# Performance work log

Measured on AMD Instinct MI355X. Metric: run time of the kernel, lower is better.

Reference implementation:

```python
import jax, jax.numpy as jnp
import numpy as np

B, T, D_IN, D_PROJ = 256, 2048, 25, 128


def setup_inputs() -> dict:
    key = jax.random.key(0)
    ks = jax.random.split(key, 7)
    s1 = 1.0 / np.sqrt(D_IN)
    s2 = 1.0 / np.sqrt(D_PROJ)
    return {
        "x": jax.random.normal(ks[0], (B, T, D_IN), dtype=jnp.float32),
        "ln_gamma": jnp.ones((D_IN,), dtype=jnp.float32),
        "ln_beta": jnp.zeros((D_IN,), dtype=jnp.float32),
        "w1": jax.random.uniform(ks[1], (D_IN, D_PROJ), jnp.float32, -s1, s1),
        "b1": jax.random.uniform(ks[2], (D_PROJ,), jnp.float32, -s1, s1),
        "w2": jax.random.uniform(ks[3], (D_PROJ, D_PROJ), jnp.float32, -s2, s2),
        "b2": jax.random.uniform(ks[4], (D_PROJ,), jnp.float32, -s2, s2),
    }


def reference(x, ln_gamma, ln_beta, w1, b1, w2, b2):
    # LayerNorm over last dim (eps=1e-5, torch default)
    mu = jnp.mean(x, axis=-1, keepdims=True)
    var = jnp.mean(jnp.square(x - mu), axis=-1, keepdims=True)
    xn = (x - mu) * jax.lax.rsqrt(var + 1e-5) * ln_gamma + ln_beta
    h = jnp.einsum("btd,dp->btp", xn, w1) + b1
    h = jax.nn.gelu(h, approximate=False)  # torch nn.GELU default = exact erf
    return jnp.einsum("btp,pq->btq", h, w2) + b2
```

## Files before the change

kernel.cpp:

```cpp
#include <hip/hip_runtime.h>
#include <hip/hip_bf16.h>
#include <stdint.h>

#define BT    (256*2048)
#define DIN   25
#define DP    128
#define MTILE 128
#define NBLK  (BT/MTILE)
#define BAND  8192
#define XOFF  4992
#define SM_BYTES (4*BAND)

typedef __attribute__((ext_vector_type(8))) __bf16 bf16x8;
typedef __attribute__((ext_vector_type(4))) __bf16 bf16x4;
typedef __attribute__((ext_vector_type(4))) float  f32x4;
typedef __attribute__((ext_vector_type(2))) float  f32x2;

__device__ __forceinline__ unsigned short f2bf(float f) {
  unsigned int u = __float_as_uint(f);
  u += 0x7fffu + ((u >> 16) & 1u);
  return (unsigned short)(u >> 16);
}

__device__ __forceinline__ float gelu_exact(float x) {
  float z  = 0.70710678118654752f * x;
  float az = __builtin_fabsf(z);
  float t  = __builtin_amdgcn_rcpf(1.0f + 0.3275911f * az);
  float p  = t*(0.254829592f + t*(-0.284496736f + t*(1.421413741f +
             t*(-1.453152027f + t*1.061405429f))));
  float e  = __expf(-z*z);
  float erf_az = 1.0f - p*e;
  float erf_z  = (x < 0.f) ? -erf_az : erf_az;
  return 0.5f * x * (1.0f + erf_z);
}

__device__ __forceinline__ void async16(void* lds, const void* g) {
  __builtin_amdgcn_global_load_lds(
      (const __attribute__((address_space(1))) unsigned int*)g,
      (__attribute__((address_space(3)))       unsigned int*)lds, 16, 0, 0);
}

__global__ void prep_kernel(const float* __restrict__ w1, const float* __restrict__ w2,
                            unsigned short* __restrict__ wf) {
  int idx = blockIdx.x * 256 + threadIdx.x;
  if (idx >= 40 * 512) return;
  int f = idx >> 9, r = idx & 511, l = r >> 3, j = r & 7;
  int l15 = l & 15, kq = (l >> 4) * 8 + j;
  float val;
  if (f < 8) {
    int n = (f >> 2) * 64 + l15 * 4 + (f & 3);
    val = (kq < DIN) ? w1[kq * DP + n] : 0.f;
  } else {
    int q = f - 8, F = q >> 2, ks = q & 3;
    int k = ks * 32 + kq;
    int n = (F >> 1) * 32 + l15 * 2 + (F & 1);
    val = w2[k * DP + n];
  }
  wf[idx] = f2bf(val);
}

__global__ __launch_bounds__(256, 3) void fused_kernel(
    const float* __restrict__ x,   const float* __restrict__ gam,
    const float* __restrict__ bet, const float* __restrict__ b1,
    const float* __restrict__ b2,  const unsigned short* __restrict__ wfr,
    float* __restrict__ out) {
  __shared__ __align__(16) unsigned char smem[SM_BYTES];
  const int tid  = threadIdx.x;
  const int lane = tid & 63, w = tid >> 6;
  const int quad = lane >> 4, l15 = lane & 15;
  const int kbase = quad * 8;
  const long long rowW = (long long)blockIdx.x * MTILE + w * 32;
  unsigned char* band = smem + w * BAND;
  const unsigned char* wfb = (const unsigned char*)wfr;

  {
    const unsigned char* src = (const unsigned char*)x + rowW * (DIN * 4);
    for (int c = lane; c < 200; c += 64)
      async16(band + XOFF + c * 16, src + c * 16);
  }

  float gk[8], bk[8];
#pragma unroll
  for (int j = 0; j < 8; j++) {
    int k = kbase + j;
    bool v = (k < DIN);
    gk[j] = v ? gam[k] : 0.f;
    bk[j] = v ? bet[k] : 0.f;
  }
  bf16x8 wb1[8];
#pragma unroll
  for (int f = 0; f < 8; f++)
    wb1[f] = *(const bf16x8*)(wfb + f * 1024 + lane * 16);
  float b1v[8];
#pragma unroll
  for (int f = 0; f < 8; f++)
    b1v[f] = b1[(f >> 2) * 64 + l15 * 4 + (f & 3)];

  asm volatile("s_waitcnt vmcnt(0)" ::: "memory");
  __builtin_amdgcn_sched_barrier(0);

  const float* xs = (const float*)(band + XOFF);
  bf16x8 afrag[2];
#pragma unroll
  for (int t = 0; t < 2; t++) {
    float xv[8];
    float s = 0.f;
#pragma unroll
    for (int j = 0; j < 8; j++) {
      int k = kbase + j;
      float v = 0.f;
      if (k < DIN) v = xs[(t * 16 + l15) * DIN + k];
      xv[j] = v;
      s += v;
    }
    s += __shfl_xor(s, 16);  s += __shfl_xor(s, 32);
    float mu = s * (1.f / DIN);
    float vv = 0.f;
#pragma unroll
    for (int j = 0; j < 8; j++) {
      int k = kbase + j;
      float d = (k < DIN) ? (xv[j] - mu) : 0.f;
      vv += d * d;
    }
    vv += __shfl_xor(vv, 16); vv += __shfl_xor(vv, 32);
    float inv = rsqrtf(vv * (1.f / DIN) + 1e-5f);
    bf16x8 av;
#pragma unroll
    for (int j = 0; j < 8; j++)
      av[j] = (__bf16)((xv[j] - mu) * inv * gk[j] + bk[j]);
    afrag[t] = av;
  }
  asm volatile("s_waitcnt lgkmcnt(0)" ::: "memory");
  __builtin_amdgcn_sched_barrier(0);

  const f32x4 zf = {0.f, 0.f, 0.f, 0.f};
#pragma unroll
  for (int t = 0; t < 2; t++) {
#pragma unroll
    for (int g = 0; g < 2; g++) {
      f32x4 acc[4];
#pragma unroll
      for (int c = 0; c < 4; c++)
        acc[c] = __builtin_amdgcn_mfma_f32_16x16x32_bf16(afrag[t], wb1[g * 4 + c], zf, 0, 0, 0);
#pragma unroll
      for (int r = 0; r < 4; r++) {
        int rl   = t * 16 + quad * 4 + r;
        int swz  = ((quad * 4 + r) & 7) << 4;
        bf16x4 hv;
#pragma unroll
        for (int c = 0; c < 4; c++)
          hv[c] = (__bf16)gelu_exact(acc[c][r] + b1v[g * 4 + c]);
        *(bf16x4*)(band + rl * 256 + ((g * 128 + l15 * 8) ^ swz)) = hv;
      }
    }
  }

  bf16x8 wb2[2][4];
#pragma unroll
  for (int ni = 0; ni < 2; ni++)
#pragma unroll
    for (int ks = 0; ks < 4; ks++)
      wb2[ni][ks] = *(const bf16x8*)(wfb + 8192 + (((w * 2 + ni) * 4) + ks) * 1024 + lane * 16);
  f32x2 bias2 = *(const f32x2*)(b2 + w * 32 + 2 * l15);

  __syncthreads();

  const long long orow0 = (long long)blockIdx.x * MTILE;
  const int rswz = (l15 & 7) << 4;
#pragma unroll
  for (int mt = 0; mt < 8; mt++) {
    bf16x8 af[4];
#pragma unroll
    for (int ks = 0; ks < 4; ks++)
      af[ks] = *(const bf16x8*)(smem + (mt * 16 + l15) * 256 + ((ks * 64 + quad * 16) ^ rswz));
    f32x4 a0 = zf, a1 = zf;
#pragma unroll
    for (int ks = 0; ks < 4; ks++) {
      a0 = __builtin_amdgcn_mfma_f32_16x16x32_bf16(af[ks], wb2[0][ks], a0, 0, 0, 0);
      a1 = __builtin_amdgcn_mfma_f32_16x16x32_bf16(af[ks], wb2[1][ks], a1, 0, 0, 0);
    }
    float* orow = out + (orow0 + mt * 16) * DP + w * 32 + 2 * l15;
#pragma unroll
    for (int r = 0; r < 4; r++) {
      int row = quad * 4 + r;
      f32x2 o; o[0] = a0[r] + bias2[0]; o[1] = a1[r] + bias2[1];
      *(f32x2*)(orow + row * DP) = o;
    }
  }
}

extern "C" void kernel_launch(void* const* d_in, const int* in_sizes, int n_in,
                              void* d_out, int out_size, void* d_ws, size_t ws_size,
                              hipStream_t stream) {
  const float* x   = (const float*)d_in[0];
  const float* gam = (const float*)d_in[1];
  const float* bet = (const float*)d_in[2];
  const float* w1  = (const float*)d_in[3];
  const float* b1  = (const float*)d_in[4];
  const float* w2  = (const float*)d_in[5];
  const float* b2  = (const float*)d_in[6];
  float* out = (float*)d_out;
  unsigned short* wf = (unsigned short*)d_ws;

  prep_kernel<<<80, 256, 0, stream>>>(w1, w2, wf);
  fused_kernel<<<NBLK, 256, 0, stream>>>(x, gam, bet, b1, b2, wf, out);
}
```

Measured before the change: 328.0 us.

## Make fused kernel persistent with double-buffered async x prefetch

Launches a fixed 1024 blocks that each loop over several 128-row tiles. The next tile's x rows are prefetched into a second LDS staging buffer with async global-to-LDS loads while the current tile runs LayerNorm, GEMM1+GELU and GEMM2. This amortizes weight fragment loads and block setup across tiles, and hides x load latency behind compute. In exchange it uses more LDS, lowers the occupancy target from 3 to 2 blocks, and adds two block barriers per tile. The wait relies on a hard-coded vmcnt(4) that must match the number of outstanding loads, including the output stores.

```diff
diff --git a/kernel.cpp b/kernel.cpp
--- a/kernel.cpp
+++ b/kernel.cpp
@@ -6,10 +6,12 @@
 #define DIN   25
 #define DP    128
 #define MTILE 128
-#define NBLK  (BT/MTILE)
-#define BAND  8192
-#define XOFF  4992
-#define SM_BYTES (4*BAND)
+#define NTILE (BT/MTILE)
+#define NBLK  1024
+#define TPB   (NTILE/NBLK)
+#define HBYTES 32768
+#define XSTG   12800
+#define SM_BYTES (HBYTES + 2*XSTG)
 
 typedef __attribute__((ext_vector_type(8))) __bf16 bf16x8;
 typedef __attribute__((ext_vector_type(4))) __bf16 bf16x4;
@@ -59,7 +61,7 @@
   wf[idx] = f2bf(val);
 }
 
-__global__ __launch_bounds__(256, 3) void fused_kernel(
+__global__ __launch_bounds__(256, 2) void fused_kernel(
     const float* __restrict__ x,   const float* __restrict__ gam,
     const float* __restrict__ bet, const float* __restrict__ b1,
     const float* __restrict__ b2,  const unsigned short* __restrict__ wfr,
@@ -69,15 +71,22 @@
   const int lane = tid & 63, w = tid >> 6;
   const int quad = lane >> 4, l15 = lane & 15;
   const int kbase = quad * 8;
-  const long long rowW = (long long)blockIdx.x * MTILE + w * 32;
-  unsigned char* band = smem + w * BAND;
+  const long long tile0 = (long long)blockIdx.x * TPB;
+  unsigned char* band = smem + w * 8192;
   const unsigned char* wfb = (const unsigned char*)wfr;
-
-  {
-    const unsigned char* src = (const unsigned char*)x + rowW * (DIN * 4);
-    for (int c = lane; c < 200; c += 64)
-      async16(band + XOFF + c * 16, src + c * 16);
-  }
+  const unsigned char* xb  = (const unsigned char*)x;
+
+  auto STAGE = [&](int ti, int sbuf) {
+    const unsigned char* src = xb + ((tile0 + ti) * 128LL + w * 32) * 100;
+    unsigned char* dst = smem + HBYTES + sbuf * XSTG + w * 3200;
+#pragma unroll
+    for (int i2 = 0; i2 < 4; i2++) {
+      int c = lane + i2 * 64;
+      if (c < 200) async16(dst + c * 16, src + c * 16);
+    }
+  };
+
+  STAGE(0, 0);
 
   float gk[8], bk[8];
 #pragma unroll
@@ -95,66 +104,6 @@
 #pragma unroll
   for (int f = 0; f < 8; f++)
     b1v[f] = b1[(f >> 2) * 64 + l15 * 4 + (f & 3)];
-
-  asm volatile("s_waitcnt vmcnt(0)" ::: "memory");
-  __builtin_amdgcn_sched_barrier(0);
-
-  const float* xs = (const float*)(band + XOFF);
-  bf16x8 afrag[2];
-#pragma unroll
-  for (int t = 0; t < 2; t++) {
-    float xv[8];
-    float s = 0.f;
-#pragma unroll
-    for (int j = 0; j < 8; j++) {
-      int k = kbase + j;
-      float v = 0.f;
-      if (k < DIN) v = xs[(t * 16 + l15) * DIN + k];
-      xv[j] = v;
-      s += v;
-    }
-    s += __shfl_xor(s, 16);  s += __shfl_xor(s, 32);
-    float mu = s * (1.f / DIN);
-    float vv = 0.f;
-#pragma unroll
-    for (int j = 0; j < 8; j++) {
-      int k = kbase + j;
-      float d = (k < DIN) ? (xv[j] - mu) : 0.f;
-      vv += d * d;
-    }
-    vv += __shfl_xor(vv, 16); vv += __shfl_xor(vv, 32);
-    float inv = rsqrtf(vv * (1.f / DIN) + 1e-5f);
-    bf16x8 av;
-#pragma unroll
-    for (int j = 0; j < 8; j++)
-      av[j] = (__bf16)((xv[j] - mu) * inv * gk[j] + bk[j]);
-    afrag[t] = av;
-  }
-  asm volatile("s_waitcnt lgkmcnt(0)" ::: "memory");
-  __builtin_amdgcn_sched_barrier(0);
-
-  const f32x4 zf = {0.f, 0.f, 0.f, 0.f};
-#pragma unroll
-  for (int t = 0; t < 2; t++) {
-#pragma unroll
-    for (int g = 0; g < 2; g++) {
-      f32x4 acc[4];
-#pragma unroll
-      for (int c = 0; c < 4; c++)
-        acc[c] = __builtin_amdgcn_mfma_f32_16x16x32_bf16(afrag[t], wb1[g * 4 + c], zf, 0, 0, 0);
-#pragma unroll
-      for (int r = 0; r < 4; r++) {
-        int rl   = t * 16 + quad * 4 + r;
-        int swz  = ((quad * 4 + r) & 7) << 4;
-        bf16x4 hv;
-#pragma unroll
-        for (int c = 0; c < 4; c++)
-          hv[c] = (__bf16)gelu_exact(acc[c][r] + b1v[g * 4 + c]);
-        *(bf16x4*)(band + rl * 256 + ((g * 128 + l15 * 8) ^ swz)) = hv;
-      }
-    }
-  }
-
   bf16x8 wb2[2][4];
 #pragma unroll
   for (int ni = 0; ni < 2; ni++)
@@ -163,29 +112,93 @@
       wb2[ni][ks] = *(const bf16x8*)(wfb + 8192 + (((w * 2 + ni) * 4) + ks) * 1024 + lane * 16);
   f32x2 bias2 = *(const f32x2*)(b2 + w * 32 + 2 * l15);
 
-  __syncthreads();
-
-  const long long orow0 = (long long)blockIdx.x * MTILE;
-  const int rswz = (l15 & 7) << 4;
-#pragma unroll
-  for (int mt = 0; mt < 8; mt++) {
-    bf16x8 af[4];
-#pragma unroll
-    for (int ks = 0; ks < 4; ks++)
-      af[ks] = *(const bf16x8*)(smem + (mt * 16 + l15) * 256 + ((ks * 64 + quad * 16) ^ rswz));
-    f32x4 a0 = zf, a1 = zf;
-#pragma unroll
-    for (int ks = 0; ks < 4; ks++) {
-      a0 = __builtin_amdgcn_mfma_f32_16x16x32_bf16(af[ks], wb2[0][ks], a0, 0, 0, 0);
-      a1 = __builtin_amdgcn_mfma_f32_16x16x32_bf16(af[ks], wb2[1][ks], a1, 0, 0, 0);
-    }
-    float* orow = out + (orow0 + mt * 16) * DP + w * 32 + 2 * l15;
-#pragma unroll
-    for (int r = 0; r < 4; r++) {
-      int row = quad * 4 + r;
-      f32x2 o; o[0] = a0[r] + bias2[0]; o[1] = a1[r] + bias2[1];
-      *(f32x2*)(orow + row * DP) = o;
-    }
+  const f32x4 zf = {0.f, 0.f, 0.f, 0.f};
+
+  for (int it = 0; it < TPB; it++) {
+    const int s = it & 1;
+    STAGE((it + 1 < TPB) ? it + 1 : 0, s ^ 1);
+    asm volatile("s_waitcnt vmcnt(4)" ::: "memory");
+    __builtin_amdgcn_sched_barrier(0);
+
+    const float* xs = (const float*)(smem + HBYTES + s * XSTG + w * 3200);
+    bf16x8 afrag[2];
+#pragma unroll
+    for (int t = 0; t < 2; t++) {
+      float xv[8];
+      float sum = 0.f;
+#pragma unroll
+      for (int j = 0; j < 8; j++) {
+        int k = kbase + j;
+        float v = 0.f;
+        if (k < DIN) v = xs[(t * 16 + l15) * DIN + k];
+        xv[j] = v;
+        sum += v;
+      }
+      sum += __shfl_xor(sum, 16);  sum += __shfl_xor(sum, 32);
+      float mu = sum * (1.f / DIN);
+      float vv = 0.f;
+#pragma unroll
+      for (int j = 0; j < 8; j++) {
+        int k = kbase + j;
+        float d = (k < DIN) ? (xv[j] - mu) : 0.f;
+        vv += d * d;
+      }
+      vv += __shfl_xor(vv, 16); vv += __shfl_xor(vv, 32);
+      float inv = rsqrtf(vv * (1.f / DIN) + 1e-5f);
+      bf16x8 av;
+#pragma unroll
+      for (int j = 0; j < 8; j++)
+        av[j] = (__bf16)((xv[j] - mu) * inv * gk[j] + bk[j]);
+      afrag[t] = av;
+    }
+
+#pragma unroll
+    for (int t = 0; t < 2; t++) {
+#pragma unroll
+      for (int cg = 0; cg < 2; cg++) {
+        f32x4 acc[4];
+#pragma unroll
+        for (int c = 0; c < 4; c++)
+          acc[c] = __builtin_amdgcn_mfma_f32_16x16x32_bf16(afrag[t], wb1[cg * 4 + c], zf, 0, 0, 0);
+#pragma unroll
+        for (int r = 0; r < 4; r++) {
+          int rl  = t * 16 + quad * 4 + r;
+          int swz = ((quad * 4 + r) & 7) << 4;
+          bf16x4 hv;
+#pragma unroll
+          for (int c = 0; c < 4; c++)
+            hv[c] = (__bf16)gelu_exact(acc[c][r] + b1v[cg * 4 + c]);
+          *(bf16x4*)(band + rl * 256 + ((cg * 128 + l15 * 8) ^ swz)) = hv;
+        }
+      }
+    }
+
+    __syncthreads();
+
+    const long long orow0 = (tile0 + it) * MTILE;
+    const int rswz = (l15 & 7) << 4;
+#pragma unroll
+    for (int mt = 0; mt < 8; mt++) {
+      bf16x8 af[4];
+#pragma unroll
+      for (int ks = 0; ks < 4; ks++)
+        af[ks] = *(const bf16x8*)(smem + (mt * 16 + l15) * 256 + ((ks * 64 + quad * 16) ^ rswz));
+      f32x4 a0 = zf, a1 = zf;
+#pragma unroll
+      for (int ks = 0; ks < 4; ks++) {
+        a0 = __builtin_amdgcn_mfma_f32_16x16x32_bf16(af[ks], wb2[0][ks], a0, 0, 0, 0);
+        a1 = __builtin_amdgcn_mfma_f32_16x16x32_bf16(af[ks], wb2[1][ks], a1, 0, 0, 0);
+      }
+      float* orow = out + (orow0 + mt * 16) * DP + w * 32 + 2 * l15;
+#pragma unroll
+      for (int r = 0; r < 4; r++) {
+        int row = quad * 4 + r;
+        f32x2 o; o[0] = a0[r] + bias2[0]; o[1] = a1[r] + bias2[1];
+        *(f32x2*)(orow + row * DP) = o;
+      }
+    }
+
+    __syncthreads();
   }
 }
 
```

Measured after the change: 330.1 us. No clear change (+0.6%).
